# Kernel tuning notes

Hardware: AMD Instinct MI355X
Metric: run time of the kernel (lower is better)

The kernel has to match this reference:

```python
import jax, jax.numpy as jnp
import numpy as np
import math

N_HEAD = 8


def _rope(x):
    # x: [B, H, S, D]; lucidrains rotary_embedding_torch default: interleaved pairs, theta=10000
    D = x.shape[-1]
    S = x.shape[-2]
    inv_freq = 1.0 / (10000.0 ** (jnp.arange(0, D, 2, dtype=jnp.float32) / D))  # [D/2]
    t = jnp.arange(S, dtype=jnp.float32)
    freqs = jnp.repeat(t[:, None] * inv_freq[None, :], 2, axis=-1)  # [S, D] interleaved repeat
    cos = jnp.cos(freqs).astype(x.dtype)
    sin = jnp.sin(freqs).astype(x.dtype)
    xp = x.reshape(*x.shape[:-1], D // 2, 2)
    rot = jnp.stack((-xp[..., 1], xp[..., 0]), axis=-1).reshape(x.shape)  # rotate_half (interleaved)
    return x * cos + rot * sin


def _row_linear(x, Wo):
    # faithful RowLinear: transpose then flat-reshape back (a real permutation), linear, inverse shuffle
    B, S, P = x.shape
    E = Wo.shape[0]
    x = jnp.swapaxes(x, 1, 2).reshape(B, S, P)
    x = jnp.einsum('bsp,ep->bse', x, Wo)  # [B, S, E]
    x = x.reshape(B, E, -1)  # [B, E, S]
    return jnp.swapaxes(x, 1, 2)  # [B, S, E]


def setup_inputs() -> dict:
    key = jax.random.key(0)
    k0, k1, k2, k3, k4 = jax.random.split(key, 5)
    B, S, E, P = 4, 2048, 1024, 1024
    std = 1.0 / math.sqrt(E)
    return {
        'emb': jax.random.normal(k0, (B, S, E), dtype=jnp.float32),
        'W1': jax.random.normal(k1, (P, E), dtype=jnp.float32) * std,
        'W2': jax.random.normal(k2, (P, E), dtype=jnp.float32) * std,
        'W3': jax.random.normal(k3, (P, E), dtype=jnp.float32) * std,
        'Wo': jax.random.normal(k4, (E, P), dtype=jnp.float32) * std,
    }


def reference(emb, W1, W2, W3, Wo):
    B, S, E = emb.shape
    P = W1.shape[0]
    H = N_HEAD
    D = P // H
    q = jnp.einsum('bse,pe->bsp', emb, W1).reshape(B, H, S, D)  # raw view split (as in source)
    k = jnp.einsum('bse,pe->bsp', emb, W2).reshape(B, H, S, D)
    v = jnp.einsum('bse,pe->bsp', emb, W3).reshape(B, H, S, D)
    q = _rope(q)
    k = _rope(k)
    scores = jnp.einsum('bhqd,bhkd->bhqk', q, k).astype(jnp.float32) / math.sqrt(H)
    attn = jax.nn.softmax(scores, axis=-1).astype(v.dtype)
    out = jnp.einsum('bhqk,bhkd->bhqd', attn, v)  # [B, H, S, D]
    out = jnp.swapaxes(out, 1, 2).reshape(B, S, P)
    return _row_linear(out, Wo)
```

## Files before the change

kernel.cpp:

```cpp
#include <hip/hip_runtime.h>

typedef float f32x4 __attribute__((ext_vector_type(4)));
typedef float f32x16 __attribute__((ext_vector_type(16)));
typedef __bf16 bf16x8 __attribute__((ext_vector_type(8)));

__device__ __forceinline__ unsigned short f2bf(float f) {
  unsigned int u = __float_as_uint(f);
  u = (u + 0x7FFFu + ((u >> 16) & 1u)) >> 16;
  return (unsigned short)u;
}

__device__ __forceinline__ f32x4 mfma16(bf16x8 a, bf16x8 b, f32x4 c) {
  return __builtin_amdgcn_mfma_f32_16x16x32_bf16(a, b, c, 0, 0, 0);
}
__device__ __forceinline__ f32x16 mfma32(bf16x8 a, bf16x8 b, f32x16 c) {
  return __builtin_amdgcn_mfma_f32_32x32x16_bf16(a, b, c, 0, 0, 0);
}

__device__ __forceinline__ unsigned int cvtpk_bf16(float a, float b) {
  unsigned int r;
  asm("v_cvt_pk_bf16_f32 %0, %1, %2" : "=v"(r) : "v"(a), "v"(b));
  return r;
}
__device__ __forceinline__ void pl32swap(unsigned int& a, unsigned int& b) {
  asm("v_permlane32_swap_b32 %0, %1" : "+v"(a), "+v"(b));
}

__device__ __forceinline__ void load8_bf16(const unsigned short* p, unsigned short* d) {
  *(uint4*)d = *(const uint4*)p;
}
__device__ __forceinline__ void load8_bf16(const float* p, unsigned short* d) {
  float4 a = *(const float4*)p;
  float4 b = *(const float4*)(p + 4);
  __align__(16) unsigned short t[8] = {f2bf(a.x), f2bf(a.y), f2bf(a.z), f2bf(a.w),
                                       f2bf(b.x), f2bf(b.y), f2bf(b.z), f2bf(b.w)};
  *(uint4*)d = *(uint4*)t;
}

__device__ __forceinline__ void gload_lds16(const unsigned short* g, unsigned short* l) {
  __builtin_amdgcn_global_load_lds(
      (const __attribute__((address_space(1))) void*)g,
      (__attribute__((address_space(3))) void*)l, 16, 0, 0);
}

__global__ __launch_bounds__(256) void convert_gen(const float* __restrict__ src,
                                                   unsigned short* __restrict__ dst) {
  int idx = (blockIdx.x * 256 + threadIdx.x) * 8;
  __align__(16) unsigned short t[8];
  load8_bf16(src + idx, t);
  *(uint4*)(dst + idx) = *(uint4*)t;
}

__global__ __launch_bounds__(256) void convert_w3(const float* __restrict__ W1,
                                                  const float* __restrict__ W2,
                                                  const float* __restrict__ W3,
                                                  unsigned short* __restrict__ dst) {
  int i = blockIdx.x;
  int sel = i >> 9;
  const float* src = (sel == 0) ? W1 : (sel == 1) ? W2 : W3;
  int off = (i & 511) * 2048 + threadIdx.x * 8;
  __align__(16) unsigned short t[8];
  load8_bf16(src + off, t);
  *(uint4*)(dst + sel * 1048576 + off) = *(uint4*)t;
}

__global__ __launch_bounds__(256) void gemm_qkv(const unsigned short* __restrict__ A,
                                                const unsigned short* __restrict__ WB,
                                                unsigned short* __restrict__ q,
                                                unsigned short* __restrict__ k,
                                                unsigned short* __restrict__ v) {
  __shared__ __align__(16) unsigned short As[128][32];
  __shared__ __align__(16) unsigned short Bs[128][32];
  const int t = threadIdx.x;
  const int lane = t & 63;
  const int wid = t >> 6;
  const int quad = lane >> 4;
  const int l16 = lane & 15;
  const int wm = (wid >> 1) << 6;
  const int wn = (wid & 1) << 6;
  const int sel = blockIdx.x >> 3;
  const int nb = (blockIdx.x & 7) << 7;
  const int mbase = blockIdx.y * 128;
  const unsigned short* Bt = WB + sel * 1048576;
  unsigned short* C = (sel == 0) ? q : (sel == 1) ? k : v;

  f32x4 acc[4][4] = {};

  for (int k0 = 0; k0 < 1024; k0 += 32) {
#pragma unroll
    for (int i = 0; i < 2; ++i) {
      int c = t + (i << 8);
      int row = c >> 2;
      int col = (c & 3) << 3;
      gload_lds16(A + (size_t)(mbase + row) * 1024 + k0 + col, &As[row][col]);
      gload_lds16(Bt + (size_t)(nb + row) * 1024 + k0 + col, &Bs[row][col]);
    }
    __syncthreads();
    bf16x8 af[4], bfr[4];
#pragma unroll
    for (int mt = 0; mt < 4; ++mt)
      af[mt] = *(const bf16x8*)(&As[wm + mt * 16 + l16][quad * 8]);
#pragma unroll
    for (int nt = 0; nt < 4; ++nt)
      bfr[nt] = *(const bf16x8*)(&Bs[wn + nt * 16 + l16][quad * 8]);
#pragma unroll
    for (int mt = 0; mt < 4; ++mt)
#pragma unroll
      for (int nt = 0; nt < 4; ++nt)
        acc[mt][nt] = mfma16(af[mt], bfr[nt], acc[mt][nt]);
    __syncthreads();
  }

  const bool rope = (sel < 2);
#pragma unroll
  for (int mt = 0; mt < 4; ++mt) {
#pragma unroll
    for (int nt = 0; nt < 4; ++nt) {
#pragma unroll
      for (int r = 0; r < 4; ++r) {
        int row_g = mbase + wm + mt * 16 + quad * 4 + r;
        int col_g = nb + wn + nt * 16 + l16;
        float val = acc[mt][nt][r];
        if (rope) {
          float other = __shfl_xor(val, 1);
          int s = (((row_g & 2047) << 3) + (col_g >> 7)) & 2047;
          int d = col_g & 127;
          float invf = __expf(-0.14391156f * (float)(d >> 1));
          float ang = (float)s * invf;
          float sv, cv;
          __sincosf(ang, &sv, &cv);
          val = (d & 1) ? (val * cv + other * sv) : (val * cv - other * sv);
        }
        C[(size_t)row_g * 1024 + col_g] = f2bf(val);
      }
    }
  }
}

__global__ __launch_bounds__(256) void transpose_v(const unsigned short* __restrict__ Vn,
                                                   unsigned short* __restrict__ VT) {
  __shared__ __align__(16) unsigned short tile[64][72];
  const int t = threadIdx.x;
  const int s0 = blockIdx.x * 64;
  const int d0 = blockIdx.y * 64;
  const int bh = blockIdx.z;
  const size_t base = (size_t)bh * (2048 * 128);
#pragma unroll
  for (int i = 0; i < 2; ++i) {
    int c = t + (i << 8);
    int sr = c >> 3;
    int dc = (c & 7) << 3;
    *(uint4*)(&tile[sr][dc]) = *(const uint4*)(Vn + base + (size_t)(s0 + sr) * 128 + d0 + dc);
  }
  __syncthreads();
#pragma unroll
  for (int i = 0; i < 2; ++i) {
    int c = t + (i << 8);
    int dr = c >> 3;
    int sc = (c & 7) << 3;
    __align__(16) unsigned short tmp[8];
#pragma unroll
    for (int j = 0; j < 8; ++j) tmp[j] = tile[sc + j][dr];
    *(uint4*)(VT + base + (size_t)(d0 + dr) * 2048 + s0 + sc) = *(uint4*)tmp;
  }
}

__global__ __launch_bounds__(256) void gemm_out(const unsigned short* __restrict__ OT,
                                                const unsigned short* __restrict__ Bt,
                                                float* __restrict__ C) {
  __shared__ __align__(16) char smem_raw[128 * 68 * 4];
  auto As = (unsigned short(*)[32])smem_raw;
  auto Bs = (unsigned short(*)[32])(smem_raw + 128 * 32 * 2);
  const int t = threadIdx.x;
  const int lane = t & 63;
  const int wid = t >> 6;
  const int quad = lane >> 4;
  const int l16 = lane & 15;
  const int wm = (wid >> 1) << 6;
  const int wn = (wid & 1) << 6;
  const int mbase = blockIdx.y * 128;
  const int nbase = blockIdx.x * 128;

  f32x4 acc[4][4] = {};

  for (int k0 = 0; k0 < 1024; k0 += 32) {
#pragma unroll
    for (int i = 0; i < 2; ++i) {
      int c = t + (i << 8);
      int row = c >> 2;
      int col = (c & 3) << 3;
      int R = mbase + row;
      int b = R >> 11;
      int ii = R & 2047;
      const unsigned short* src = OT + (size_t)(b * 8 + (ii >> 8)) * (128 * 2048) +
                                  (size_t)((ii >> 1) & 127) * 2048 + ((ii & 1) << 10) +
                                  k0 + col;
      gload_lds16(src, &As[row][col]);
      gload_lds16(Bt + (size_t)(nbase + row) * 1024 + k0 + col, &Bs[row][col]);
    }
    __syncthreads();
    bf16x8 af[4], bfr[4];
#pragma unroll
    for (int mt = 0; mt < 4; ++mt)
      af[mt] = *(const bf16x8*)(&As[wm + mt * 16 + l16][quad * 8]);
#pragma unroll
    for (int nt = 0; nt < 4; ++nt)
      bfr[nt] = *(const bf16x8*)(&Bs[wn + nt * 16 + l16][quad * 8]);
#pragma unroll
    for (int mt = 0; mt < 4; ++mt)
#pragma unroll
      for (int nt = 0; nt < 4; ++nt)
        acc[mt][nt] = mfma16(af[mt], bfr[nt], acc[mt][nt]);
    __syncthreads();
  }

  float(*Ts)[68] = (float(*)[68])smem_raw;
  const int b = mbase >> 11;
  const int ebase = (mbase & 2047) >> 1;
#pragma unroll
  for (int p = 0; p < 2; ++p) {
    __syncthreads();
#pragma unroll
    for (int mt = 0; mt < 4; ++mt)
#pragma unroll
      for (int nt = 0; nt < 4; ++nt)
#pragma unroll
        for (int rr = p; rr < 4; rr += 2) {
          int col_local = wn + nt * 16 + l16;
          int row_local = wm + mt * 16 + quad * 4 + rr;
          Ts[col_local][row_local >> 1] = acc[mt][nt][rr];
        }
    __syncthreads();
    int srow = t >> 1;
    int e0 = (t & 1) << 5;
    float* dst = C + (size_t)b * 2097152 +
                 (size_t)(p * 1024 + nbase + srow) * 1024 + ebase + e0;
#pragma unroll
    for (int j = 0; j < 8; ++j)
      ((float4*)dst)[j] = *(const float4*)&Ts[srow][e0 + j * 4];
  }
}

__global__ __launch_bounds__(256, 2) void flash_attn(const unsigned short* __restrict__ Q,
                                                     const unsigned short* __restrict__ Kg,
                                                     const unsigned short* __restrict__ VTg,
                                                     unsigned short* __restrict__ OT) {
  __shared__ __align__(16) char sm[65536];
  const int t = threadIdx.x;
  const int lane = t & 63;
  const int wid = t >> 6;
  const int l31 = lane & 31;
  const int hi = lane >> 5;
  const int x16 = (l31 & 7) << 4;
  const int i = blockIdx.x;
  const int bh = (i & 7) + ((i >> 3) & 3) * 8;
  const int qbase = (i >> 5) << 7;
  const size_t base = (size_t)bh * (2048 * 128);
  const float scale = 0.3535533905932738f;

  bf16x8 qf[8];
  {
    const unsigned short* qp = Q + base + (size_t)(qbase + wid * 32 + l31) * 128 + hi * 8;
#pragma unroll
    for (int ks = 0; ks < 8; ++ks) qf[ks] = *(const bf16x8*)(qp + ks * 16);
  }

  f32x16 accO[4] = {};
  float m = -__builtin_inff();
  float l = 0.f;

  uint4 kreg[4], vreg[4];
  const unsigned short* Kg_b = Kg + base;
  const unsigned short* Vg_b = VTg + base;

#pragma unroll
  for (int j = 0; j < 4; ++j) {
    int c = t + (j << 8);
    kreg[j] = *(const uint4*)(Kg_b + (size_t)(c >> 4) * 128 + ((c & 15) << 3));
    vreg[j] = *(const uint4*)(Vg_b + (size_t)(c >> 3) * 2048 + ((c & 7) << 3));
  }
  {
    unsigned short* Kw = (unsigned short*)sm;
    unsigned short* Vw = (unsigned short*)(sm + 16384);
#pragma unroll
    for (int j = 0; j < 4; ++j) {
      int c = t + (j << 8);
      int r = c >> 4, ch = c & 15;
      *(uint4*)(Kw + r * 128 + ((ch ^ (r & 7)) << 3)) = kreg[j];
      int d = c >> 3, cv = c & 7;
      *(uint4*)(Vw + d * 64 + ((cv ^ (d & 7)) << 3)) = vreg[j];
    }
  }
  __syncthreads();

  int cur = 0;
  for (int kv = 0; kv < 2048; kv += 64) {
    const bool nxt = (kv + 64) < 2048;
    if (nxt) {
#pragma unroll
      for (int j = 0; j < 4; ++j) {
        int c = t + (j << 8);
        kreg[j] = *(const uint4*)(Kg_b + (size_t)(kv + 64 + (c >> 4)) * 128 + ((c & 15) << 3));
        vreg[j] = *(const uint4*)(Vg_b + (size_t)(c >> 3) * 2048 + (kv + 64) + ((c & 7) << 3));
      }
    }
    const char* Kb = sm + (cur << 15);
    const char* Vb = Kb + 16384;

    f32x16 s0 = {}, s1 = {};
#pragma unroll
    for (int ks = 0; ks < 8; ++ks) {
      int cb = (ks * 32 + hi * 16) ^ x16;
      bf16x8 k0 = *(const bf16x8*)(Kb + l31 * 256 + cb);
      bf16x8 k1 = *(const bf16x8*)(Kb + 8192 + l31 * 256 + cb);
      s0 = mfma32(k0, qf[ks], s0);
      s1 = mfma32(k1, qf[ks], s1);
    }

    float mx = s0[0];
#pragma unroll
    for (int r = 1; r < 16; ++r) mx = fmaxf(mx, s0[r]);
#pragma unroll
    for (int r = 0; r < 16; ++r) mx = fmaxf(mx, s1[r]);
    mx = fmaxf(mx, __shfl_xor(mx, 32));
    if (__any(mx > m + 16.f)) {
      float mnew = fmaxf(m, mx);
      float alpha = __expf((m - mnew) * scale);
      l *= alpha;
#pragma unroll
      for (int dt = 0; dt < 4; ++dt)
#pragma unroll
        for (int r = 0; r < 16; ++r) accO[dt][r] *= alpha;
      m = mnew;
    }
    float negms = -m * scale;
    float ps = 0.f;
#pragma unroll
    for (int r = 0; r < 16; ++r) {
      s0[r] = __expf(fmaf(s0[r], scale, negms));
      ps += s0[r];
    }
#pragma unroll
    for (int r = 0; r < 16; ++r) {
      s1[r] = __expf(fmaf(s1[r], scale, negms));
      ps += s1[r];
    }
    ps += __shfl_xor(ps, 32);
    l += ps;

    bf16x8 pfrag[4];
#pragma unroll
    for (int kb = 0; kb < 4; ++kb) {
      const f32x16& S = (kb < 2) ? s0 : s1;
      const int b = (kb & 1) * 8;
      unsigned int a0 = cvtpk_bf16(S[b + 0], S[b + 1]);
      unsigned int a1 = cvtpk_bf16(S[b + 2], S[b + 3]);
      unsigned int a2 = cvtpk_bf16(S[b + 4], S[b + 5]);
      unsigned int a3 = cvtpk_bf16(S[b + 6], S[b + 7]);
      pl32swap(a0, a2);
      pl32swap(a1, a3);
      union { unsigned int u[4]; bf16x8 v; } pu;
      pu.u[0] = a0; pu.u[1] = a1; pu.u[2] = a2; pu.u[3] = a3;
      pfrag[kb] = pu.v;
    }

#pragma unroll
    for (int dt = 0; dt < 4; ++dt) {
#pragma unroll
      for (int kb = 0; kb < 4; ++kb) {
        bf16x8 vfr = *(const bf16x8*)(Vb + l31 * 128 + dt * 4096 + ((kb * 32 + hi * 16) ^ x16));
        accO[dt] = mfma32(vfr, pfrag[kb], accO[dt]);
      }
    }

    if (nxt) {
      unsigned short* Kw = (unsigned short*)(sm + ((cur ^ 1) << 15));
      unsigned short* Vw = (unsigned short*)((char*)Kw + 16384);
#pragma unroll
      for (int j = 0; j < 4; ++j) {
        int c = t + (j << 8);
        int r = c >> 4, ch = c & 15;
        *(uint4*)(Kw + r * 128 + ((ch ^ (r & 7)) << 3)) = kreg[j];
        int d = c >> 3, cv = c & 7;
        *(uint4*)(Vw + d * 64 + ((cv ^ (d & 7)) << 3)) = vreg[j];
      }
    }
    __syncthreads();
    cur ^= 1;
  }

  auto To = (unsigned short(*)[136])sm;
  const float invl = 1.f / l;
  const int qloc = wid * 32 + l31;
#pragma unroll
  for (int dt = 0; dt < 4; ++dt)
#pragma unroll
    for (int r = 0; r < 16; ++r) {
      int d = dt * 32 + (r & 3) + ((r >> 2) << 3) + hi * 4;
      To[d][qloc] = f2bf(accO[dt][r] * invl);
    }
  __syncthreads();
  int dr = t >> 1;
  int off = (t & 1) << 6;
  unsigned short* dst = OT + base + (size_t)dr * 2048 + qbase + off;
#pragma unroll
  for (int j = 0; j < 8; ++j)
    ((uint4*)dst)[j] = *(const uint4*)&To[dr][off + j * 8];
}

extern "C" void kernel_launch(void* const* d_in, const int* in_sizes, int n_in,
                              void* d_out, int out_size, void* d_ws, size_t ws_size,
                              hipStream_t stream) {
  const float* emb = (const float*)d_in[0];
  const float* W1  = (const float*)d_in[1];
  const float* W2  = (const float*)d_in[2];
  const float* W3  = (const float*)d_in[3];
  const float* Wo  = (const float*)d_in[4];
  float* out = (float*)d_out;

  const size_t NELEM = (size_t)8 * 1024 * 1024;
  unsigned short* q     = (unsigned short*)d_ws;
  unsigned short* k     = q + NELEM;
  unsigned short* vn    = k + NELEM;
  unsigned short* X     = vn + NELEM;
  unsigned short* oT    = vn;
  unsigned short* vT    = X;
  unsigned short* W123B = X;
  unsigned short* WoB   = X;
  unsigned short* embB  = (unsigned short*)d_out;

  dim3 blk(256, 1, 1);
  convert_w3<<<dim3(1536), blk, 0, stream>>>(W1, W2, W3, W123B);
  convert_gen<<<dim3(4096), blk, 0, stream>>>(emb, embB);
  gemm_qkv<<<dim3(24, 64), blk, 0, stream>>>(embB, W123B, q, k, vn);
  transpose_v<<<dim3(32, 2, 32), blk, 0, stream>>>(vn, vT);
  flash_attn<<<dim3(512, 1, 1), blk, 0, stream>>>(q, k, vT, oT);
  convert_gen<<<dim3(512), blk, 0, stream>>>(Wo, WoB);
  gemm_out<<<dim3(8, 64), blk, 0, stream>>>(oT, WoB, out);
}
```

Measured before the change: 365.2 us.

## Split flash attention over two KV halves and merge partial outputs

Flash attention now splits each query tile's KV range into two halves (split-K), doubling the grid to 1024 blocks. Each half writes a partial bf16 output plus its running max and sum. Two small kernels then compute the merge weights and combine the partials. The KV tiles are loaded with direct global-to-LDS loads into a single buffer, replacing register-staged double buffering, which cuts shared memory and raises the occupancy target to 4 blocks per CU. The max and sum reductions are also rewritten as trees. In exchange it adds extra launches, extra global traffic for the partials, extra bf16 rounding of the partial outputs, and exposed load latency behind two barriers per iteration.

```diff
diff --git a/kernel.cpp b/kernel.cpp
--- a/kernel.cpp
+++ b/kernel.cpp
@@ -8,6 +8,9 @@
   unsigned int u = __float_as_uint(f);
   u = (u + 0x7FFFu + ((u >> 16) & 1u)) >> 16;
   return (unsigned short)u;
+}
+__device__ __forceinline__ float bf2f(unsigned short u) {
+  return __uint_as_float((unsigned int)u << 16);
 }
 
 __device__ __forceinline__ f32x4 mfma16(bf16x8 a, bf16x8 b, f32x4 c) {
@@ -241,11 +244,14 @@
   }
 }
 
-__global__ __launch_bounds__(256, 2) void flash_attn(const unsigned short* __restrict__ Q,
+__global__ __launch_bounds__(256, 4) void flash_attn(const unsigned short* __restrict__ Q,
                                                      const unsigned short* __restrict__ Kg,
                                                      const unsigned short* __restrict__ VTg,
-                                                     unsigned short* __restrict__ OT) {
-  __shared__ __align__(16) char sm[65536];
+                                                     unsigned short* __restrict__ PO0,
+                                                     unsigned short* __restrict__ PO1,
+                                                     float2* __restrict__ ML0,
+                                                     float2* __restrict__ ML1) {
+  __shared__ __align__(16) char sm[34816];
   const int t = threadIdx.x;
   const int lane = t & 63;
   const int wid = t >> 6;
@@ -254,9 +260,17 @@
   const int x16 = (l31 & 7) << 4;
   const int i = blockIdx.x;
   const int bh = (i & 7) + ((i >> 3) & 3) * 8;
-  const int qbase = (i >> 5) << 7;
+  const int half = (i >> 5) & 1;
+  const int qbase = (i >> 6) << 7;
+  const int kv_lo = half << 10;
+  const int kv_hi = kv_lo + 1024;
   const size_t base = (size_t)bh * (2048 * 128);
   const float scale = 0.3535533905932738f;
+
+  unsigned short* PO = half ? PO1 : PO0;
+  float2* ML = half ? ML1 : ML0;
+  unsigned short* Ks_lin = (unsigned short*)sm;
+  unsigned short* Vs_lin = (unsigned short*)(sm + 16384);
 
   bf16x8 qf[8];
   {
@@ -269,43 +283,24 @@
   float m = -__builtin_inff();
   float l = 0.f;
 
-  uint4 kreg[4], vreg[4];
   const unsigned short* Kg_b = Kg + base;
   const unsigned short* Vg_b = VTg + base;
 
 #pragma unroll
   for (int j = 0; j < 4; ++j) {
     int c = t + (j << 8);
-    kreg[j] = *(const uint4*)(Kg_b + (size_t)(c >> 4) * 128 + ((c & 15) << 3));
-    vreg[j] = *(const uint4*)(Vg_b + (size_t)(c >> 3) * 2048 + ((c & 7) << 3));
-  }
-  {
-    unsigned short* Kw = (unsigned short*)sm;
-    unsigned short* Vw = (unsigned short*)(sm + 16384);
-#pragma unroll
-    for (int j = 0; j < 4; ++j) {
-      int c = t + (j << 8);
-      int r = c >> 4, ch = c & 15;
-      *(uint4*)(Kw + r * 128 + ((ch ^ (r & 7)) << 3)) = kreg[j];
-      int d = c >> 3, cv = c & 7;
-      *(uint4*)(Vw + d * 64 + ((cv ^ (d & 7)) << 3)) = vreg[j];
-    }
+    int row = c >> 4, ch = c & 15;
+    gload_lds16(Kg_b + (size_t)(kv_lo + row) * 128 + ((ch ^ (row & 7)) << 3),
+                Ks_lin + c * 8);
+    int d = c >> 3, cv = c & 7;
+    gload_lds16(Vg_b + (size_t)d * 2048 + kv_lo + ((cv ^ (d & 7)) << 3),
+                Vs_lin + c * 8);
   }
   __syncthreads();
 
-  int cur = 0;
-  for (int kv = 0; kv < 2048; kv += 64) {
-    const bool nxt = (kv + 64) < 2048;
-    if (nxt) {
-#pragma unroll
-      for (int j = 0; j < 4; ++j) {
-        int c = t + (j << 8);
-        kreg[j] = *(const uint4*)(Kg_b + (size_t)(kv + 64 + (c >> 4)) * 128 + ((c & 15) << 3));
-        vreg[j] = *(const uint4*)(Vg_b + (size_t)(c >> 3) * 2048 + (kv + 64) + ((c & 7) << 3));
-      }
-    }
-    const char* Kb = sm + (cur << 15);
-    const char* Vb = Kb + 16384;
+  for (int kv = kv_lo; kv < kv_hi; kv += 64) {
+    const char* Kb = sm;
+    const char* Vb = sm + 16384;
 
     f32x16 s0 = {}, s1 = {};
 #pragma unroll
@@ -317,12 +312,14 @@
       s1 = mfma32(k1, qf[ks], s1);
     }
 
-    float mx = s0[0];
-#pragma unroll
-    for (int r = 1; r < 16; ++r) mx = fmaxf(mx, s0[r]);
-#pragma unroll
-    for (int r = 0; r < 16; ++r) mx = fmaxf(mx, s1[r]);
-    mx = fmaxf(mx, __shfl_xor(mx, 32));
+    float tm[16];
+#pragma unroll
+    for (int r = 0; r < 16; ++r) tm[r] = fmaxf(s0[r], s1[r]);
+#pragma unroll
+    for (int d = 8; d > 0; d >>= 1)
+#pragma unroll
+      for (int r = 0; r < d; ++r) tm[r] = fmaxf(tm[r], tm[r + d]);
+    float mx = fmaxf(tm[0], __shfl_xor(tm[0], 32));
     if (__any(mx > m + 16.f)) {
       float mnew = fmaxf(m, mx);
       float alpha = __expf((m - mnew) * scale);
@@ -334,19 +331,18 @@
       m = mnew;
     }
     float negms = -m * scale;
-    float ps = 0.f;
-#pragma unroll
-    for (int r = 0; r < 16; ++r) {
-      s0[r] = __expf(fmaf(s0[r], scale, negms));
-      ps += s0[r];
-    }
-#pragma unroll
-    for (int r = 0; r < 16; ++r) {
-      s1[r] = __expf(fmaf(s1[r], scale, negms));
-      ps += s1[r];
-    }
-    ps += __shfl_xor(ps, 32);
-    l += ps;
+#pragma unroll
+    for (int r = 0; r < 16; ++r) s0[r] = __expf(fmaf(s0[r], scale, negms));
+#pragma unroll
+    for (int r = 0; r < 16; ++r) s1[r] = __expf(fmaf(s1[r], scale, negms));
+    float ts[16];
+#pragma unroll
+    for (int r = 0; r < 16; ++r) ts[r] = s0[r] + s1[r];
+#pragma unroll
+    for (int d = 8; d > 0; d >>= 1)
+#pragma unroll
+      for (int r = 0; r < d; ++r) ts[r] += ts[r + d];
+    l += ts[0] + __shfl_xor(ts[0], 32);
 
     bf16x8 pfrag[4];
 #pragma unroll
@@ -373,20 +369,20 @@
       }
     }
 
-    if (nxt) {
-      unsigned short* Kw = (unsigned short*)(sm + ((cur ^ 1) << 15));
-      unsigned short* Vw = (unsigned short*)((char*)Kw + 16384);
+    __syncthreads();
+    if (kv + 64 < kv_hi) {
 #pragma unroll
       for (int j = 0; j < 4; ++j) {
         int c = t + (j << 8);
-        int r = c >> 4, ch = c & 15;
-        *(uint4*)(Kw + r * 128 + ((ch ^ (r & 7)) << 3)) = kreg[j];
+        int row = c >> 4, ch = c & 15;
+        gload_lds16(Kg_b + (size_t)(kv + 64 + row) * 128 + ((ch ^ (row & 7)) << 3),
+                    Ks_lin + c * 8);
         int d = c >> 3, cv = c & 7;
-        *(uint4*)(Vw + d * 64 + ((cv ^ (d & 7)) << 3)) = vreg[j];
+        gload_lds16(Vg_b + (size_t)d * 2048 + (kv + 64) + ((cv ^ (d & 7)) << 3),
+                    Vs_lin + c * 8);
       }
     }
     __syncthreads();
-    cur ^= 1;
   }
 
   auto To = (unsigned short(*)[136])sm;
@@ -399,13 +395,53 @@
       int d = dt * 32 + (r & 3) + ((r >> 2) << 3) + hi * 4;
       To[d][qloc] = f2bf(accO[dt][r] * invl);
     }
+  if (hi == 0) {
+    float2 v; v.x = m; v.y = l;
+    ML[bh * 2048 + qbase + qloc] = v;
+  }
   __syncthreads();
   int dr = t >> 1;
   int off = (t & 1) << 6;
-  unsigned short* dst = OT + base + (size_t)dr * 2048 + qbase + off;
+  unsigned short* dst = PO + base + (size_t)dr * 2048 + qbase + off;
 #pragma unroll
   for (int j = 0; j < 8; ++j)
     ((uint4*)dst)[j] = *(const uint4*)&To[dr][off + j * 8];
+}
+
+__global__ __launch_bounds__(256) void attn_mweights(const float2* __restrict__ ml0,
+                                                     const float2* __restrict__ ml1,
+                                                     float2* __restrict__ w) {
+  int idx = blockIdx.x * 256 + threadIdx.x;
+  float2 a = ml0[idx];
+  float2 b = ml1[idx];
+  float mm = fmaxf(a.x, b.x);
+  float e0 = a.y * __expf((a.x - mm) * 0.3535533905932738f);
+  float e1 = b.y * __expf((b.x - mm) * 0.3535533905932738f);
+  float inv = 1.f / (e0 + e1);
+  float2 o; o.x = e0 * inv; o.y = e1 * inv;
+  w[idx] = o;
+}
+
+__global__ __launch_bounds__(256) void attn_merge(const unsigned short* __restrict__ P0,
+                                                  const unsigned short* __restrict__ P1,
+                                                  const float2* __restrict__ w,
+                                                  unsigned short* __restrict__ O) {
+  size_t idx = ((size_t)blockIdx.x * 256 + threadIdx.x) * 8;
+  int s = (int)(idx & 2047);
+  int bh = (int)(idx >> 18);
+  uint4 a0 = *(const uint4*)(P0 + idx);
+  uint4 a1 = *(const uint4*)(P1 + idx);
+  const unsigned short* u0 = (const unsigned short*)&a0;
+  const unsigned short* u1 = (const unsigned short*)&a1;
+  const float4* wp = (const float4*)(w + ((size_t)bh << 11) + s);
+  float2 ww[8];
+#pragma unroll
+  for (int j = 0; j < 4; ++j) *(float4*)&ww[j * 2] = wp[j];
+  __align__(16) unsigned short o[8];
+#pragma unroll
+  for (int j = 0; j < 8; ++j)
+    o[j] = f2bf(fmaf(ww[j].x, bf2f(u0[j]), ww[j].y * bf2f(u1[j])));
+  *(uint4*)(O + idx) = *(const uint4*)o;
 }
 
 extern "C" void kernel_launch(void* const* d_in, const int* in_sizes, int n_in,
@@ -428,13 +464,19 @@
   unsigned short* W123B = X;
   unsigned short* WoB   = X;
   unsigned short* embB  = (unsigned short*)d_out;
+  unsigned short* P1  = (unsigned short*)d_out;
+  float2* ml0 = (float2*)((char*)d_out + (size_t)(16 << 20));
+  float2* ml1 = (float2*)((char*)d_out + (size_t)(16 << 20) + (512 << 10));
+  float2* wbf = (float2*)((char*)d_out + (size_t)(17 << 20));
 
   dim3 blk(256, 1, 1);
   convert_w3<<<dim3(1536), blk, 0, stream>>>(W1, W2, W3, W123B);
   convert_gen<<<dim3(4096), blk, 0, stream>>>(emb, embB);
   gemm_qkv<<<dim3(24, 64), blk, 0, stream>>>(embB, W123B, q, k, vn);
   transpose_v<<<dim3(32, 2, 32), blk, 0, stream>>>(vn, vT);
-  flash_attn<<<dim3(512, 1, 1), blk, 0, stream>>>(q, k, vT, oT);
+  flash_attn<<<dim3(1024, 1, 1), blk, 0, stream>>>(q, k, vT, oT, P1, ml0, ml1);
+  attn_mweights<<<dim3(256), blk, 0, stream>>>(ml0, ml1, wbf);
+  attn_merge<<<dim3(4096), blk, 0, stream>>>(oT, P1, wbf, oT);
   convert_gen<<<dim3(512), blk, 0, stream>>>(Wo, WoB);
   gemm_out<<<dim3(8, 64), blk, 0, stream>>>(oT, WoB, out);
 }
```

Result: slower. 417.6 us (+14.4%).

## Double-buffer GEMM and attention tiles with direct global-to-LDS loads

Applied to the files above, without the earlier changes.

Both GEMM kernels gain a second LDS buffer: the next K tile is prefetched with global_load_lds while the current tile feeds the MFMAs, and each iteration ends with a single vmcnt drain plus barrier instead of two syncthreads. The attention kernel drops register staging of K/V and writes them straight into swizzled double-buffered LDS via global_load_lds, moving the XOR swizzle to the source address. Softmax max and sum reductions become tree reductions to shorten dependency chains. The cost is more LDS per block, which may lower occupancy, and the full vmcnt drain each iteration can still expose load latency.

```diff
diff --git a/kernel.cpp b/kernel.cpp
--- a/kernel.cpp
+++ b/kernel.cpp
@@ -8,6 +8,9 @@
   unsigned int u = __float_as_uint(f);
   u = (u + 0x7FFFu + ((u >> 16) & 1u)) >> 16;
   return (unsigned short)u;
+}
+__device__ __forceinline__ float bf2f(unsigned short u) {
+  return __uint_as_float((unsigned int)u << 16);
 }
 
 __device__ __forceinline__ f32x4 mfma16(bf16x8 a, bf16x8 b, f32x4 c) {
@@ -41,6 +44,13 @@
   __builtin_amdgcn_global_load_lds(
       (const __attribute__((address_space(1))) void*)g,
       (__attribute__((address_space(3))) void*)l, 16, 0, 0);
+}
+
+__device__ __forceinline__ void drain_barrier() {
+  asm volatile("s_waitcnt vmcnt(0)" ::: "memory");
+  __builtin_amdgcn_sched_barrier(0);
+  __builtin_amdgcn_s_barrier();
+  __builtin_amdgcn_sched_barrier(0);
 }
 
 __global__ __launch_bounds__(256) void convert_gen(const float* __restrict__ src,
@@ -69,8 +79,8 @@
                                                 unsigned short* __restrict__ q,
                                                 unsigned short* __restrict__ k,
                                                 unsigned short* __restrict__ v) {
-  __shared__ __align__(16) unsigned short As[128][32];
-  __shared__ __align__(16) unsigned short Bs[128][32];
+  __shared__ __align__(16) unsigned short As[2][128][32];
+  __shared__ __align__(16) unsigned short Bs[2][128][32];
   const int t = threadIdx.x;
   const int lane = t & 63;
   const int wid = t >> 6;
@@ -86,29 +96,36 @@
 
   f32x4 acc[4][4] = {};
 
-  for (int k0 = 0; k0 < 1024; k0 += 32) {
+  auto stage = [&](int k0, int p) {
 #pragma unroll
     for (int i = 0; i < 2; ++i) {
       int c = t + (i << 8);
       int row = c >> 2;
       int col = (c & 3) << 3;
-      gload_lds16(A + (size_t)(mbase + row) * 1024 + k0 + col, &As[row][col]);
-      gload_lds16(Bt + (size_t)(nb + row) * 1024 + k0 + col, &Bs[row][col]);
-    }
-    __syncthreads();
+      gload_lds16(A + (size_t)(mbase + row) * 1024 + k0 + col, &As[p][row][col]);
+      gload_lds16(Bt + (size_t)(nb + row) * 1024 + k0 + col, &Bs[p][row][col]);
+    }
+  };
+
+  stage(0, 0);
+  drain_barrier();
+
+  for (int k0 = 0; k0 < 1024; k0 += 32) {
+    const int p = (k0 >> 5) & 1;
+    if (k0 + 32 < 1024) stage(k0 + 32, p ^ 1);
     bf16x8 af[4], bfr[4];
 #pragma unroll
     for (int mt = 0; mt < 4; ++mt)
-      af[mt] = *(const bf16x8*)(&As[wm + mt * 16 + l16][quad * 8]);
+      af[mt] = *(const bf16x8*)(&As[p][wm + mt * 16 + l16][quad * 8]);
 #pragma unroll
     for (int nt = 0; nt < 4; ++nt)
-      bfr[nt] = *(const bf16x8*)(&Bs[wn + nt * 16 + l16][quad * 8]);
+      bfr[nt] = *(const bf16x8*)(&Bs[p][wn + nt * 16 + l16][quad * 8]);
 #pragma unroll
     for (int mt = 0; mt < 4; ++mt)
 #pragma unroll
       for (int nt = 0; nt < 4; ++nt)
         acc[mt][nt] = mfma16(af[mt], bfr[nt], acc[mt][nt]);
-    __syncthreads();
+    drain_barrier();
   }
 
   const bool rope = (sel < 2);
@@ -169,8 +186,6 @@
                                                 const unsigned short* __restrict__ Bt,
                                                 float* __restrict__ C) {
   __shared__ __align__(16) char smem_raw[128 * 68 * 4];
-  auto As = (unsigned short(*)[32])smem_raw;
-  auto Bs = (unsigned short(*)[32])(smem_raw + 128 * 32 * 2);
   const int t = threadIdx.x;
   const int lane = t & 63;
   const int wid = t >> 6;
@@ -183,7 +198,9 @@
 
   f32x4 acc[4][4] = {};
 
-  for (int k0 = 0; k0 < 1024; k0 += 32) {
+  auto stage = [&](int k0, int p) {
+    auto As = (unsigned short(*)[32])(smem_raw + p * 16384);
+    auto Bs = (unsigned short(*)[32])(smem_raw + p * 16384 + 8192);
 #pragma unroll
     for (int i = 0; i < 2; ++i) {
       int c = t + (i << 8);
@@ -198,7 +215,16 @@
       gload_lds16(src, &As[row][col]);
       gload_lds16(Bt + (size_t)(nbase + row) * 1024 + k0 + col, &Bs[row][col]);
     }
-    __syncthreads();
+  };
+
+  stage(0, 0);
+  drain_barrier();
+
+  for (int k0 = 0; k0 < 1024; k0 += 32) {
+    const int p = (k0 >> 5) & 1;
+    if (k0 + 32 < 1024) stage(k0 + 32, p ^ 1);
+    auto As = (unsigned short(*)[32])(smem_raw + p * 16384);
+    auto Bs = (unsigned short(*)[32])(smem_raw + p * 16384 + 8192);
     bf16x8 af[4], bfr[4];
 #pragma unroll
     for (int mt = 0; mt < 4; ++mt)
@@ -211,7 +237,7 @@
 #pragma unroll
       for (int nt = 0; nt < 4; ++nt)
         acc[mt][nt] = mfma16(af[mt], bfr[nt], acc[mt][nt]);
-    __syncthreads();
+    drain_barrier();
   }
 
   float(*Ts)[68] = (float(*)[68])smem_raw;
@@ -258,6 +284,23 @@
   const size_t base = (size_t)bh * (2048 * 128);
   const float scale = 0.3535533905932738f;
 
+  const unsigned short* Kg_b = Kg + base;
+  const unsigned short* Vg_b = VTg + base;
+
+  auto issueKV = [&](int kvoff, int pbit) {
+    unsigned short* Kl = (unsigned short*)(sm + (pbit << 14));
+    unsigned short* Vl = (unsigned short*)(sm + 32768 + (pbit << 14));
+#pragma unroll
+    for (int j = 0; j < 4; ++j) {
+      int c = t + (j << 8);
+      int row = c >> 4, ch = c & 15;
+      gload_lds16(Kg_b + (size_t)(kvoff + row) * 128 + ((ch ^ (row & 7)) << 3),
+                  Kl + c * 8);
+      int d = c >> 3, cv = c & 7;
+      gload_lds16(Vg_b + (size_t)d * 2048 + kvoff + ((cv ^ (d & 7)) << 3), Vl + c * 8);
+    }
+  };
+
   bf16x8 qf[8];
   {
     const unsigned short* qp = Q + base + (size_t)(qbase + wid * 32 + l31) * 128 + hi * 8;
@@ -269,43 +312,14 @@
   float m = -__builtin_inff();
   float l = 0.f;
 
-  uint4 kreg[4], vreg[4];
-  const unsigned short* Kg_b = Kg + base;
-  const unsigned short* Vg_b = VTg + base;
-
-#pragma unroll
-  for (int j = 0; j < 4; ++j) {
-    int c = t + (j << 8);
-    kreg[j] = *(const uint4*)(Kg_b + (size_t)(c >> 4) * 128 + ((c & 15) << 3));
-    vreg[j] = *(const uint4*)(Vg_b + (size_t)(c >> 3) * 2048 + ((c & 7) << 3));
-  }
-  {
-    unsigned short* Kw = (unsigned short*)sm;
-    unsigned short* Vw = (unsigned short*)(sm + 16384);
-#pragma unroll
-    for (int j = 0; j < 4; ++j) {
-      int c = t + (j << 8);
-      int r = c >> 4, ch = c & 15;
-      *(uint4*)(Kw + r * 128 + ((ch ^ (r & 7)) << 3)) = kreg[j];
-      int d = c >> 3, cv = c & 7;
-      *(uint4*)(Vw + d * 64 + ((cv ^ (d & 7)) << 3)) = vreg[j];
-    }
-  }
-  __syncthreads();
-
-  int cur = 0;
+  issueKV(0, 0);
+  drain_barrier();
+
   for (int kv = 0; kv < 2048; kv += 64) {
-    const bool nxt = (kv + 64) < 2048;
-    if (nxt) {
-#pragma unroll
-      for (int j = 0; j < 4; ++j) {
-        int c = t + (j << 8);
-        kreg[j] = *(const uint4*)(Kg_b + (size_t)(kv + 64 + (c >> 4)) * 128 + ((c & 15) << 3));
-        vreg[j] = *(const uint4*)(Vg_b + (size_t)(c >> 3) * 2048 + (kv + 64) + ((c & 7) << 3));
-      }
-    }
-    const char* Kb = sm + (cur << 15);
-    const char* Vb = Kb + 16384;
+    const int p = (kv >> 6) & 1;
+    if (kv + 64 < 2048) issueKV(kv + 64, p ^ 1);
+    const char* Kb = sm + (p << 14);
+    const char* Vb = sm + 32768 + (p << 14);
 
     f32x16 s0 = {}, s1 = {};
 #pragma unroll
@@ -317,12 +331,15 @@
       s1 = mfma32(k1, qf[ks], s1);
     }
 
-    float mx = s0[0];
-#pragma unroll
-    for (int r = 1; r < 16; ++r) mx = fmaxf(mx, s0[r]);
-#pragma unroll
-    for (int r = 0; r < 16; ++r) mx = fmaxf(mx, s1[r]);
-    mx = fmaxf(mx, __shfl_xor(mx, 32));
+    float t8[8];
+#pragma unroll
+    for (int r = 0; r < 8; ++r)
+      t8[r] = fmaxf(fmaxf(s0[r], s0[r + 8]), fmaxf(s1[r], s1[r + 8]));
+#pragma unroll
+    for (int d = 4; d > 0; d >>= 1)
+#pragma unroll
+      for (int r = 0; r < d; ++r) t8[r] = fmaxf(t8[r], t8[r + d]);
+    float mx = fmaxf(t8[0], __shfl_xor(t8[0], 32));
     if (__any(mx > m + 16.f)) {
       float mnew = fmaxf(m, mx);
       float alpha = __expf((m - mnew) * scale);
@@ -334,19 +351,18 @@
       m = mnew;
     }
     float negms = -m * scale;
-    float ps = 0.f;
-#pragma unroll
-    for (int r = 0; r < 16; ++r) {
-      s0[r] = __expf(fmaf(s0[r], scale, negms));
-      ps += s0[r];
-    }
-#pragma unroll
-    for (int r = 0; r < 16; ++r) {
-      s1[r] = __expf(fmaf(s1[r], scale, negms));
-      ps += s1[r];
-    }
-    ps += __shfl_xor(ps, 32);
-    l += ps;
+#pragma unroll
+    for (int r = 0; r < 16; ++r) s0[r] = __expf(fmaf(s0[r], scale, negms));
+#pragma unroll
+    for (int r = 0; r < 16; ++r) s1[r] = __expf(fmaf(s1[r], scale, negms));
+#pragma unroll
+    for (int r = 0; r < 8; ++r)
+      t8[r] = (s0[r] + s0[r + 8]) + (s1[r] + s1[r + 8]);
+#pragma unroll
+    for (int d = 4; d > 0; d >>= 1)
+#pragma unroll
+      for (int r = 0; r < d; ++r) t8[r] += t8[r + d];
+    l += t8[0] + __shfl_xor(t8[0], 32);
 
     bf16x8 pfrag[4];
 #pragma unroll
@@ -368,25 +384,13 @@
     for (int dt = 0; dt < 4; ++dt) {
 #pragma unroll
       for (int kb = 0; kb < 4; ++kb) {
-        bf16x8 vfr = *(const bf16x8*)(Vb + l31 * 128 + dt * 4096 + ((kb * 32 + hi * 16) ^ x16));
+        bf16x8 vfr = *(const bf16x8*)(Vb + l31 * 128 + dt * 4096 +
+                                      ((kb * 32 + hi * 16) ^ x16));
         accO[dt] = mfma32(vfr, pfrag[kb], accO[dt]);
       }
     }
 
-    if (nxt) {
-      unsigned short* Kw = (unsigned short*)(sm + ((cur ^ 1) << 15));
-      unsigned short* Vw = (unsigned short*)((char*)Kw + 16384);
-#pragma unroll
-      for (int j = 0; j < 4; ++j) {
-        int c = t + (j << 8);
-        int r = c >> 4, ch = c & 15;
-        *(uint4*)(Kw + r * 128 + ((ch ^ (r & 7)) << 3)) = kreg[j];
-        int d = c >> 3, cv = c & 7;
-        *(uint4*)(Vw + d * 64 + ((cv ^ (d & 7)) << 3)) = vreg[j];
-      }
-    }
-    __syncthreads();
-    cur ^= 1;
+    drain_barrier();
   }
 
   auto To = (unsigned short(*)[136])sm;
```

After: 318.7 us. -12.7%, faster.
